# Kernel tuning notes

Measured on AMD Instinct MI355X. Metric: run time of the kernel, lower is better.

Reference implementation:

```python
import jax, jax.numpy as jnp
import numpy as np

NUM_USERS = 100000
NUM_ITEMS = 50000
D = 64
NUM_LAYERS = 2
NNZ_H = 3200000
NNZ_I = 3000000
EPS = 1e-12


def setup_inputs() -> dict:
    key = jax.random.key(0)
    ks = jax.random.split(key, 24)
    inp = {}
    inp['user_emb'] = jax.random.normal(ks[0], (NUM_USERS, D), jnp.float32) * 0.1
    inp['item_emb'] = jax.random.normal(ks[1], (NUM_ITEMS, D), jnp.float32) * 0.1
    inp['gating_w'] = jax.random.normal(ks[2], (4, D, D), jnp.float32) * 0.1
    inp['gating_b'] = jax.random.normal(ks[3], (4, 1, D), jnp.float32) * 0.1
    inp['sgating_w'] = jax.random.normal(ks[4], (3, D, D), jnp.float32) * 0.1
    inp['sgating_b'] = jax.random.normal(ks[5], (3, 1, D), jnp.float32) * 0.1
    inp['att_mat'] = jax.random.normal(ks[6], (D, D), jnp.float32) * 0.1
    inp['att_agg'] = jax.random.normal(ks[7], (1, D), jnp.float32) * 0.1
    inp['hs_row'] = jax.random.randint(ks[8], (NNZ_H,), 0, NUM_USERS, jnp.int32)
    inp['hs_col'] = jax.random.randint(ks[9], (NNZ_H,), 0, NUM_USERS, jnp.int32)
    inp['hs_val'] = jax.random.uniform(ks[10], (NNZ_H,), jnp.float32) / 32.0
    inp['hj_row'] = jax.random.randint(ks[11], (NNZ_H,), 0, NUM_USERS, jnp.int32)
    inp['hj_col'] = jax.random.randint(ks[12], (NNZ_H,), 0, NUM_USERS, jnp.int32)
    inp['hj_val'] = jax.random.uniform(ks[13], (NNZ_H,), jnp.float32) / 32.0
    inp['hp_row'] = jax.random.randint(ks[14], (NNZ_H,), 0, NUM_USERS, jnp.int32)
    inp['hp_col'] = jax.random.randint(ks[15], (NNZ_H,), 0, NUM_USERS, jnp.int32)
    inp['hp_val'] = jax.random.uniform(ks[16], (NNZ_H,), jnp.float32) / 32.0
    inp['inter_row'] = jax.random.randint(ks[17], (NNZ_I,), 0, NUM_USERS, jnp.int32)
    inp['inter_col'] = jax.random.randint(ks[18], (NNZ_I,), 0, NUM_ITEMS, jnp.int32)
    inp['inter_val'] = jax.random.uniform(ks[19], (NNZ_I,), jnp.float32) / 32.0
    return inp


def spmm(row, col, val, x, n_rows):
    # sparse (n_rows x m) @ dense (m x d), COO edges
    return jax.ops.segment_sum(val[:, None] * x[col], row, num_segments=n_rows)


def l2norm(x):
    return x / jnp.maximum(jnp.linalg.norm(x, axis=1, keepdims=True), EPS)


def self_gating(em, w, b):
    return em * jax.nn.sigmoid(em @ w + b)


def channel_attention(embs, att_mat, att_agg):
    # embs: list of 3 arrays [N, D]
    w = jnp.stack([jnp.sum(att_agg * (e @ att_mat), axis=1) for e in embs])  # [3, N]
    score = jax.nn.softmax(w, axis=0)
    mixed = score[0][:, None] * embs[0] + score[1][:, None] * embs[1] + score[2][:, None] * embs[2]
    return mixed, score


def reference(user_emb, item_emb, gating_w, gating_b, sgating_w, sgating_b,
              att_mat, att_agg,
              hs_row, hs_col, hs_val, hj_row, hj_col, hj_val,
              hp_row, hp_col, hp_val, inter_row, inter_col, inter_val):
    u_c0 = self_gating(user_emb, gating_w[0], gating_b[0])
    u_c1 = self_gating(user_emb, gating_w[1], gating_b[1])
    u_c2 = self_gating(user_emb, gating_w[2], gating_b[2])
    u_simple = self_gating(user_emb, gating_w[3], gating_b[3])
    it = item_emb
    acc_c0, acc_c1, acc_c2 = u_c0, u_c1, u_c2
    acc_simple, acc_item = u_simple, it
    for _ in range(NUM_LAYERS):
        mixed, _ = channel_attention([u_c0, u_c1, u_c2], att_mat, att_agg)
        mixed = (mixed + u_simple) / 2.0
        u_c0 = spmm(hs_row, hs_col, hs_val, u_c0, NUM_USERS)
        acc_c0 = acc_c0 + l2norm(u_c0)
        u_c1 = spmm(hj_row, hj_col, hj_val, u_c1, NUM_USERS)
        acc_c1 = acc_c1 + l2norm(u_c1)
        u_c2 = spmm(hp_row, hp_col, hp_val, u_c2, NUM_USERS)
        acc_c2 = acc_c2 + l2norm(u_c2)
        new_item = spmm(inter_col, inter_row, inter_val, mixed, NUM_ITEMS)  # inter^T @ mixed
        acc_item = acc_item + l2norm(new_item)
        u_simple = spmm(inter_row, inter_col, inter_val, it, NUM_USERS)  # inter @ item (old)
        acc_simple = acc_simple + l2norm(u_simple)
        it = new_item
    final_user, _ = channel_attention([acc_c0, acc_c1, acc_c2], att_mat, att_agg)
    final_user = final_user + acc_simple / 2.0
    sg0 = self_gating(final_user, sgating_w[0], sgating_b[0])
    sg1 = self_gating(final_user, sgating_w[1], sgating_b[1])
    sg2 = self_gating(final_user, sgating_w[2], sgating_b[2])
    return final_user, acc_item, sg0, sg1, sg2
```

## Files before the change

kernel.cpp:

```cpp
#include <hip/hip_runtime.h>

#define D 64
#define EPS 1e-12f

#define SB 6
#define BSZ (1 << SB)
#define NBMAX 2048
#define NCHUNK 128

__device__ __forceinline__ float wave_sum(float v) {
#pragma unroll
  for (int off = 32; off > 0; off >>= 1) v += __shfl_xor(v, off, 64);
  return v;
}

__global__ void compute_v_kernel(const float* __restrict__ att_mat,
                                 const float* __restrict__ att_agg,
                                 float* __restrict__ v) {
  int d = threadIdx.x;
  float s = 0.f;
#pragma unroll
  for (int j = 0; j < D; ++j) s += att_mat[d * D + j] * att_agg[j];
  v[d] = s;
}

__global__ __launch_bounds__(256) void gating4_kernel(
    const float* __restrict__ emb, const float* __restrict__ W,
    const float* __restrict__ B, float* __restrict__ u0, float* __restrict__ u1,
    float* __restrict__ u2, float* __restrict__ u3, float* __restrict__ a0,
    float* __restrict__ a1, float* __restrict__ a2, float* __restrict__ a3,
    int nrows) {
  __shared__ float sW[4 * D * D];
  for (int i = threadIdx.x; i < 4 * D * D; i += blockDim.x) sW[i] = W[i];
  __syncthreads();
  int lane = threadIdx.x & 63;
  int wid = (blockIdx.x * blockDim.x + threadIdx.x) >> 6;
  int nw = (gridDim.x * blockDim.x) >> 6;
  float b0 = B[0 * D + lane], b1 = B[1 * D + lane];
  float b2 = B[2 * D + lane], b3 = B[3 * D + lane];
  for (int r = wid; r < nrows; r += nw) {
    float e = emb[r * D + lane];
    float y0 = b0, y1 = b1, y2 = b2, y3 = b3;
#pragma unroll 16
    for (int j = 0; j < D; ++j) {
      float ej = __shfl(e, j, 64);
      y0 += ej * sW[0 * D * D + j * D + lane];
      y1 += ej * sW[1 * D * D + j * D + lane];
      y2 += ej * sW[2 * D * D + j * D + lane];
      y3 += ej * sW[3 * D * D + j * D + lane];
    }
    float o0 = e / (1.f + __expf(-y0));
    float o1 = e / (1.f + __expf(-y1));
    float o2 = e / (1.f + __expf(-y2));
    float o3 = e / (1.f + __expf(-y3));
    int idx = r * D + lane;
    u0[idx] = o0; a0[idx] = o0;
    u1[idx] = o1; a1[idx] = o1;
    u2[idx] = o2; a2[idx] = o2;
    u3[idx] = o3; a3[idx] = o3;
  }
}

__global__ __launch_bounds__(256) void sgating3_kernel(
    const float* __restrict__ x, const float* __restrict__ W,
    const float* __restrict__ B, float* __restrict__ o0f,
    float* __restrict__ o1f, float* __restrict__ o2f, int nrows) {
  __shared__ float sW[3 * D * D];
  for (int i = threadIdx.x; i < 3 * D * D; i += blockDim.x) sW[i] = W[i];
  __syncthreads();
  int lane = threadIdx.x & 63;
  int wid = (blockIdx.x * blockDim.x + threadIdx.x) >> 6;
  int nw = (gridDim.x * blockDim.x) >> 6;
  float b0 = B[0 * D + lane], b1 = B[1 * D + lane], b2 = B[2 * D + lane];
  for (int r = wid; r < nrows; r += nw) {
    float e = x[r * D + lane];
    float y0 = b0, y1 = b1, y2 = b2;
#pragma unroll 16
    for (int j = 0; j < D; ++j) {
      float ej = __shfl(e, j, 64);
      y0 += ej * sW[0 * D * D + j * D + lane];
      y1 += ej * sW[1 * D * D + j * D + lane];
      y2 += ej * sW[2 * D * D + j * D + lane];
    }
    int idx = r * D + lane;
    o0f[idx] = e / (1.f + __expf(-y0));
    o1f[idx] = e / (1.f + __expf(-y1));
    o2f[idx] = e / (1.f + __expf(-y2));
  }
}

__global__ __launch_bounds__(256) void attn_mix_kernel(
    const float* __restrict__ u0, const float* __restrict__ u1,
    const float* __restrict__ u2, const float* __restrict__ us,
    const float* __restrict__ v, float* __restrict__ mixed, int nrows) {
  int lane = threadIdx.x & 63;
  int wid = (blockIdx.x * blockDim.x + threadIdx.x) >> 6;
  if (wid >= nrows) return;
  int idx = wid * D + lane;
  float e0 = u0[idx], e1 = u1[idx], e2 = u2[idx], eu = us[idx];
  float vd = v[lane];
  float w0 = wave_sum(e0 * vd);
  float w1 = wave_sum(e1 * vd);
  float w2 = wave_sum(e2 * vd);
  float m = fmaxf(w0, fmaxf(w1, w2));
  float s0 = __expf(w0 - m), s1 = __expf(w1 - m), s2 = __expf(w2 - m);
  float inv = 1.f / (s0 + s1 + s2);
  mixed[idx] = ((s0 * e0 + s1 * e1 + s2 * e2) * inv + eu) * 0.5f;
}

__global__ __launch_bounds__(256) void final_attn_kernel(
    const float* __restrict__ a0, const float* __restrict__ a1,
    const float* __restrict__ a2, const float* __restrict__ as,
    const float* __restrict__ v, float* __restrict__ out, int nrows) {
  int lane = threadIdx.x & 63;
  int wid = (blockIdx.x * blockDim.x + threadIdx.x) >> 6;
  if (wid >= nrows) return;
  int idx = wid * D + lane;
  float e0 = a0[idx], e1 = a1[idx], e2 = a2[idx], eu = as[idx];
  float vd = v[lane];
  float w0 = wave_sum(e0 * vd);
  float w1 = wave_sum(e1 * vd);
  float w2 = wave_sum(e2 * vd);
  float m = fmaxf(w0, fmaxf(w1, w2));
  float s0 = __expf(w0 - m), s1 = __expf(w1 - m), s2 = __expf(w2 - m);
  float inv = 1.f / (s0 + s1 + s2);
  out[idx] = (s0 * e0 + s1 * e1 + s2 * e2) * inv + 0.5f * eu;
}

__global__ __launch_bounds__(256) void l2acc_kernel(const float* __restrict__ x,
                                                    float* __restrict__ acc,
                                                    int nrows) {
  int lane = threadIdx.x & 63;
  int wid = (blockIdx.x * blockDim.x + threadIdx.x) >> 6;
  if (wid >= nrows) return;
  int idx = wid * D + lane;
  float xv = x[idx];
  float ss = wave_sum(xv * xv);
  float nrm = fmaxf(sqrtf(ss), EPS);
  acc[idx] += xv / nrm;
}

__global__ __launch_bounds__(256) void spmm_atomic_kernel(
    const int* __restrict__ row, const int* __restrict__ col,
    const float* __restrict__ val, const float* __restrict__ x,
    float* __restrict__ out, int nnz) {
  int lane = threadIdx.x & 63;
  int wid = (blockIdx.x * blockDim.x + threadIdx.x) >> 6;
  int nw = (gridDim.x * blockDim.x) >> 6;
  for (int base = wid * 64; base < nnz; base += nw * 64) {
    int e = base + lane;
    int r = 0, c = 0;
    float v = 0.f;
    if (e < nnz) { r = row[e]; c = col[e]; v = val[e]; }
    int cnt = nnz - base; if (cnt > 64) cnt = 64;
    for (int i = 0; i < cnt; ++i) {
      int ri = __shfl(r, i, 64);
      int ci = __shfl(c, i, 64);
      float vi = __shfl(v, i, 64);
      float xv = x[ci * D + lane];
      atomicAdd(&out[ri * D + lane], vi * xv);
    }
  }
}


__global__ __launch_bounds__(256) void hist_kernel(const int* __restrict__ row,
                                                   int* __restrict__ counts,
                                                   int nnz) {
  int i = blockIdx.x * blockDim.x + threadIdx.x;
  int n = gridDim.x * blockDim.x;
  for (; i < nnz; i += n) atomicAdd(&counts[row[i]], 1);
}

__global__ __launch_bounds__(256) void scan1_kernel(const int* __restrict__ in,
                                                    int* __restrict__ out,
                                                    int* __restrict__ partials,
                                                    int n) {
  __shared__ int lds[256];
  int t = threadIdx.x;
  int base = blockIdx.x * 2048 + t * 8;
  int v[8];
  int s = 0;
#pragma unroll
  for (int k = 0; k < 8; ++k) {
    int i = base + k;
    v[k] = (i < n) ? in[i] : 0;
    s += v[k];
  }
  lds[t] = s;
  __syncthreads();
  for (int ofs = 1; ofs < 256; ofs <<= 1) {
    int add = 0;
    if (t >= ofs) add = lds[t - ofs];
    __syncthreads();
    if (t >= ofs) lds[t] += add;
    __syncthreads();
  }
  int excl = lds[t] - s;
  if (t == 255) partials[blockIdx.x] = lds[255];
  int run = excl;
#pragma unroll
  for (int k = 0; k < 8; ++k) {
    int i = base + k;
    if (i < n) out[i] = run;
    run += v[k];
  }
}

__global__ __launch_bounds__(256) void scan2_kernel(int* __restrict__ partials,
                                                    int P) {
  __shared__ int lds[256];
  int t = threadIdx.x;
  int s = (t < P) ? partials[t] : 0;
  lds[t] = s;
  __syncthreads();
  for (int ofs = 1; ofs < 256; ofs <<= 1) {
    int add = 0;
    if (t >= ofs) add = lds[t - ofs];
    __syncthreads();
    if (t >= ofs) lds[t] += add;
    __syncthreads();
  }
  if (t < P) partials[t] = lds[t] - s;
}

__global__ __launch_bounds__(256) void scan3_kernel(
    int* __restrict__ out, const int* __restrict__ partials, int n) {
  int i = blockIdx.x * blockDim.x + threadIdx.x;
  int nt = gridDim.x * blockDim.x;
  for (; i < n; i += nt) out[i] += partials[i >> 11];
}

__global__ __launch_bounds__(256) void bhist_kernel(
    const int* __restrict__ row, int* __restrict__ bh, int nnz, int nb,
    int chunk) {
  __shared__ int hist[NBMAX];
  for (int i = threadIdx.x; i < nb; i += blockDim.x) hist[i] = 0;
  __syncthreads();
  int base = blockIdx.x * chunk;
  int lim = base + chunk;
  if (lim > nnz) lim = nnz;
  for (int e = base + threadIdx.x; e < lim; e += blockDim.x)
    atomicAdd(&hist[row[e] >> SB], 1);
  __syncthreads();
  int* o = bh + blockIdx.x * nb;
  for (int i = threadIdx.x; i < nb; i += blockDim.x) o[i] = hist[i];
}

__global__ __launch_bounds__(256) void bscan_kernel(
    const int* __restrict__ row_ptr, int* __restrict__ bh, int nb) {
  int b = blockIdx.x * blockDim.x + threadIdx.x;
  if (b >= nb) return;
  int run = row_ptr[b << SB];
#pragma unroll 4
  for (int k = 0; k < NCHUNK; ++k) {
    int idx = k * nb + b;
    int t = bh[idx];
    bh[idx] = run;
    run += t;
  }
}

__global__ __launch_bounds__(256) void bscatter_kernel(
    const int* __restrict__ row, const int* __restrict__ col,
    const float* __restrict__ val, const int* __restrict__ bh,
    int2* __restrict__ staging, int nnz, int nb, int chunk) {
  __shared__ int cur[NBMAX];
  const int* o = bh + blockIdx.x * nb;
  for (int i = threadIdx.x; i < nb; i += blockDim.x) cur[i] = o[i];
  __syncthreads();
  int base = blockIdx.x * chunk;
  int lim = base + chunk;
  if (lim > nnz) lim = nnz;
  for (int e = base + threadIdx.x; e < lim; e += blockDim.x) {
    int r = row[e];
    int b = r >> SB;
    int idx = atomicAdd(&cur[b], 1);
    staging[idx] =
        make_int2(((r & (BSZ - 1)) << 24) | col[e], __float_as_int(val[e]));
  }
}

__global__ __launch_bounds__(256) void bucket_scatter_kernel(
    const int* __restrict__ row_ptr, const int2* __restrict__ staging,
    int2* __restrict__ edges_out, int nrows) {
  __shared__ int lfill[BSZ];
  int b = blockIdx.x;
  int r0 = b << SB;
  int t = threadIdx.x;
  int rend = r0 + BSZ;
  if (rend > nrows) rend = nrows;
  if (t < BSZ) {
    int r = r0 + t;
    lfill[t] = row_ptr[r < nrows ? r : nrows];
  }
  int bstart = row_ptr[r0];
  int bend = row_ptr[rend];
  __syncthreads();
  for (int e = bstart + t; e < bend; e += blockDim.x) {
    int2 ev = staging[e];
    int lrow = ((unsigned)ev.x) >> 24;
    int idx = atomicAdd(&lfill[lrow], 1);
    edges_out[idx] = make_int2(ev.x & 0xFFFFFF, ev.y);
  }
}

__global__ __launch_bounds__(256) void spmm_csr_l2acc_kernel(
    const int* __restrict__ row_ptr, const int2* __restrict__ edges,
    const float* __restrict__ x, float* __restrict__ out,
    float* __restrict__ acc, int nrows) {
  int lane = threadIdx.x & 63;
  int r = (blockIdx.x * blockDim.x + threadIdx.x) >> 6;
  if (r >= nrows) return;
  int start = row_ptr[r], end = row_ptr[r + 1];
  float sum = 0.f;
  for (int j = start; j < end; j += 64) {
    int e = j + lane;
    int c = 0;
    float v = 0.f;
    if (e < end) {
      int2 ev = edges[e];
      c = ev.x;
      v = __int_as_float(ev.y);
    }
    int cnt = end - j;
    if (cnt > 64) cnt = 64;
    int i = 0;
    for (; i + 4 <= cnt; i += 4) {
      int c0 = __shfl(c, i, 64);
      int c1 = __shfl(c, i + 1, 64);
      int c2 = __shfl(c, i + 2, 64);
      int c3 = __shfl(c, i + 3, 64);
      float v0 = __shfl(v, i, 64);
      float v1 = __shfl(v, i + 1, 64);
      float v2 = __shfl(v, i + 2, 64);
      float v3 = __shfl(v, i + 3, 64);
      float x0 = x[c0 * D + lane];
      float x1 = x[c1 * D + lane];
      float x2 = x[c2 * D + lane];
      float x3 = x[c3 * D + lane];
      sum += v0 * x0;
      sum += v1 * x1;
      sum += v2 * x2;
      sum += v3 * x3;
    }
    for (; i < cnt; ++i) {
      int ci = __shfl(c, i, 64);
      float vi = __shfl(v, i, 64);
      sum += vi * x[ci * D + lane];
    }
  }
  int idx = r * D + lane;
  out[idx] = sum;
  float ss = wave_sum(sum * sum);
  float nrm = fmaxf(sqrtf(ss), EPS);
  acc[idx] += sum / nrm;
}


static void build_csr(const int* row, const int* col, const float* val, int nnz,
                      int nrows, int* counts, int* row_ptr, int* partials,
                      int* bh, int2* staging, int2* edges_out,
                      hipStream_t stream) {
  int n1 = nrows + 1;
  hipMemsetAsync(counts, 0, n1 * sizeof(int), stream);
  hipLaunchKernelGGL(hist_kernel, dim3(1024), dim3(256), 0, stream, row, counts,
                     nnz);
  int nblk = (n1 + 2047) / 2048;
  hipLaunchKernelGGL(scan1_kernel, dim3(nblk), dim3(256), 0, stream, counts,
                     row_ptr, partials, n1);
  hipLaunchKernelGGL(scan2_kernel, dim3(1), dim3(256), 0, stream, partials,
                     nblk);
  hipLaunchKernelGGL(scan3_kernel, dim3(64), dim3(256), 0, stream, row_ptr,
                     partials, n1);
  int nb = (nrows + BSZ - 1) >> SB;
  int chunk = (nnz + NCHUNK - 1) / NCHUNK;
  hipLaunchKernelGGL(bhist_kernel, dim3(NCHUNK), dim3(256), 0, stream, row, bh,
                     nnz, nb, chunk);
  hipLaunchKernelGGL(bscan_kernel, dim3((nb + 255) / 256), dim3(256), 0, stream,
                     row_ptr, bh, nb);
  hipLaunchKernelGGL(bscatter_kernel, dim3(NCHUNK), dim3(256), 0, stream, row,
                     col, val, bh, staging, nnz, nb, chunk);
  hipLaunchKernelGGL(bucket_scatter_kernel, dim3(nb), dim3(256), 0, stream,
                     row_ptr, staging, edges_out, nrows);
}

extern "C" void kernel_launch(void* const* d_in, const int* in_sizes, int n_in,
                              void* d_out, int out_size, void* d_ws,
                              size_t ws_size, hipStream_t stream) {
  const float* user_emb = (const float*)d_in[0];
  const float* item_emb = (const float*)d_in[1];
  const float* gating_w = (const float*)d_in[2];
  const float* gating_b = (const float*)d_in[3];
  const float* sgating_w = (const float*)d_in[4];
  const float* sgating_b = (const float*)d_in[5];
  const float* att_mat = (const float*)d_in[6];
  const float* att_agg = (const float*)d_in[7];
  const int* hs_row = (const int*)d_in[8];
  const int* hs_col = (const int*)d_in[9];
  const float* hs_val = (const float*)d_in[10];
  const int* hj_row = (const int*)d_in[11];
  const int* hj_col = (const int*)d_in[12];
  const float* hj_val = (const float*)d_in[13];
  const int* hp_row = (const int*)d_in[14];
  const int* hp_col = (const int*)d_in[15];
  const float* hp_val = (const float*)d_in[16];
  const int* inter_row = (const int*)d_in[17];
  const int* inter_col = (const int*)d_in[18];
  const float* inter_val = (const float*)d_in[19];

  const int U = in_sizes[0] / D;
  const int I = in_sizes[1] / D;
  const int NH = in_sizes[8];
  const int NI = in_sizes[17];
  const size_t UD = (size_t)U * D;
  const size_t ID = (size_t)I * D;

  float* out = (float*)d_out;
  float* final_user = out;
  float* acc_item = out + UD;
  float* sg0 = out + UD + ID;
  float* sg1 = sg0 + UD;
  float* sg2 = sg1 + UD;
  float* acc0 = sg0, *acc1 = sg1, *acc2 = sg2, *accS = final_user;

  char* p = (char*)d_ws;
  auto alloc = [&](size_t bytes) -> void* {
    void* r = (void*)p;
    p += (bytes + 255) & ~(size_t)255;
    return r;
  };
  float* u0 = (float*)alloc(UD * 4);
  float* u1 = (float*)alloc(UD * 4);
  float* u2 = (float*)alloc(UD * 4);
  float* us = (float*)alloc(UD * 4);
  float* mixed = (float*)alloc(UD * 4);
  float* spare = (float*)alloc(UD * 4);
  float* it_a = (float*)alloc(ID * 4);
  float* it_b = (float*)alloc(ID * 4);
  float* v = (float*)alloc(256 * 4);
  int* partials = (int*)alloc(256 * 4);
  int* cnt_u = (int*)alloc((U + 2) * 4);
  int* cnt_i = (int*)alloc((I + 2) * 4);
  int* bh = (int*)alloc((size_t)NCHUNK * NBMAX * 4);
  int* rp_hs = (int*)alloc((U + 2) * 4);
  int* rp_hj = (int*)alloc((U + 2) * 4);
  int* rp_hp = (int*)alloc((U + 2) * 4);
  int* rp_iu = (int*)alloc((U + 2) * 4);
  int* rp_ii = (int*)alloc((I + 2) * 4);
  size_t NMAX = (size_t)(NH > NI ? NH : NI);
  int2* staging;
  if (NMAX * 8 <= UD * 4) staging = (int2*)spare;
  else staging = (int2*)alloc(NMAX * 8);
  int2* ed_hs = (int2*)alloc((size_t)NH * 8);
  int2* ed_hj = (int2*)alloc((size_t)NH * 8);
  int2* ed_hp = (int2*)alloc((size_t)NH * 8);
  int2* ed_iu = (int2*)alloc((size_t)NI * 8);
  int2* ed_ii = (int2*)alloc((size_t)NI * 8);
  size_t needed = (size_t)(p - (char*)d_ws);
  bool use_csr = needed <= ws_size && U < (1 << 24) && I < (1 << 24) &&
                 U <= NBMAX * BSZ && I <= NBMAX * BSZ;

  const int ROWB_U = (U + 3) / 4;
  const int ROWB_I = (I + 3) / 4;
  const int SPMM_BLOCKS = 2048;

  hipLaunchKernelGGL(compute_v_kernel, dim3(1), dim3(64), 0, stream, att_mat,
                     att_agg, v);
  hipLaunchKernelGGL(gating4_kernel, dim3(512), dim3(256), 0, stream, user_emb,
                     gating_w, gating_b, u0, u1, u2, us, acc0, acc1, acc2, accS,
                     U);
  hipMemcpyAsync(acc_item, item_emb, ID * sizeof(float),
                 hipMemcpyDeviceToDevice, stream);
  hipMemcpyAsync(it_a, item_emb, ID * sizeof(float), hipMemcpyDeviceToDevice,
                 stream);

  if (use_csr) {
    build_csr(hs_row, hs_col, hs_val, NH, U, cnt_u, rp_hs, partials, bh,
              staging, ed_hs, stream);
    build_csr(hj_row, hj_col, hj_val, NH, U, cnt_u, rp_hj, partials, bh,
              staging, ed_hj, stream);
    build_csr(hp_row, hp_col, hp_val, NH, U, cnt_u, rp_hp, partials, bh,
              staging, ed_hp, stream);
    build_csr(inter_row, inter_col, inter_val, NI, U, cnt_u, rp_iu, partials,
              bh, staging, ed_iu, stream);
    build_csr(inter_col, inter_row, inter_val, NI, I, cnt_i, rp_ii, partials,
              bh, staging, ed_ii, stream);
  }

  float* it_old = it_a;
  float* it_new = it_b;

  for (int layer = 0; layer < 2; ++layer) {
    hipLaunchKernelGGL(attn_mix_kernel, dim3(ROWB_U), dim3(256), 0, stream, u0,
                       u1, u2, us, v, mixed, U);
    if (use_csr) {
      hipLaunchKernelGGL(spmm_csr_l2acc_kernel, dim3(ROWB_U), dim3(256), 0,
                         stream, rp_hs, ed_hs, u0, spare, acc0, U);
      { float* t = u0; u0 = spare; spare = t; }
      hipLaunchKernelGGL(spmm_csr_l2acc_kernel, dim3(ROWB_U), dim3(256), 0,
                         stream, rp_hj, ed_hj, u1, spare, acc1, U);
      { float* t = u1; u1 = spare; spare = t; }
      hipLaunchKernelGGL(spmm_csr_l2acc_kernel, dim3(ROWB_U), dim3(256), 0,
                         stream, rp_hp, ed_hp, u2, spare, acc2, U);
      { float* t = u2; u2 = spare; spare = t; }
      hipLaunchKernelGGL(spmm_csr_l2acc_kernel, dim3(ROWB_I), dim3(256), 0,
                         stream, rp_ii, ed_ii, mixed, it_new, acc_item, I);
      hipLaunchKernelGGL(spmm_csr_l2acc_kernel, dim3(ROWB_U), dim3(256), 0,
                         stream, rp_iu, ed_iu, it_old, spare, accS, U);
      { float* t = us; us = spare; spare = t; }
    } else {
      hipMemsetAsync(spare, 0, UD * sizeof(float), stream);
      hipLaunchKernelGGL(spmm_atomic_kernel, dim3(SPMM_BLOCKS), dim3(256), 0,
                         stream, hs_row, hs_col, hs_val, u0, spare, NH);
      hipLaunchKernelGGL(l2acc_kernel, dim3(ROWB_U), dim3(256), 0, stream,
                         spare, acc0, U);
      { float* t = u0; u0 = spare; spare = t; }
      hipMemsetAsync(spare, 0, UD * sizeof(float), stream);
      hipLaunchKernelGGL(spmm_atomic_kernel, dim3(SPMM_BLOCKS), dim3(256), 0,
                         stream, hj_row, hj_col, hj_val, u1, spare, NH);
      hipLaunchKernelGGL(l2acc_kernel, dim3(ROWB_U), dim3(256), 0, stream,
                         spare, acc1, U);
      { float* t = u1; u1 = spare; spare = t; }
      hipMemsetAsync(spare, 0, UD * sizeof(float), stream);
      hipLaunchKernelGGL(spmm_atomic_kernel, dim3(SPMM_BLOCKS), dim3(256), 0,
                         stream, hp_row, hp_col, hp_val, u2, spare, NH);
      hipLaunchKernelGGL(l2acc_kernel, dim3(ROWB_U), dim3(256), 0, stream,
                         spare, acc2, U);
      { float* t = u2; u2 = spare; spare = t; }
      hipMemsetAsync(it_new, 0, ID * sizeof(float), stream);
      hipLaunchKernelGGL(spmm_atomic_kernel, dim3(SPMM_BLOCKS), dim3(256), 0,
                         stream, inter_col, inter_row, inter_val, mixed, it_new,
                         NI);
      hipLaunchKernelGGL(l2acc_kernel, dim3(ROWB_I), dim3(256), 0, stream,
                         it_new, acc_item, I);
      hipMemsetAsync(spare, 0, UD * sizeof(float), stream);
      hipLaunchKernelGGL(spmm_atomic_kernel, dim3(SPMM_BLOCKS), dim3(256), 0,
                         stream, inter_row, inter_col, inter_val, it_old, spare,
                         NI);
      hipLaunchKernelGGL(l2acc_kernel, dim3(ROWB_U), dim3(256), 0, stream,
                         spare, accS, U);
      { float* t = us; us = spare; spare = t; }
    }
    { float* t = it_old; it_old = it_new; it_new = t; }
  }

  hipLaunchKernelGGL(final_attn_kernel, dim3(ROWB_U), dim3(256), 0, stream,
                     acc0, acc1, acc2, accS, v, final_user, U);
  hipLaunchKernelGGL(sgating3_kernel, dim3(512), dim3(256), 0, stream,
                     final_user, sgating_w, sgating_b, sg0, sg1, sg2, U);
}
```

Before: 3.434 ms.

## Batch gating rows with float4 weights and skip accumulator init copies

The gating and self-gating kernels now process four rows per wave and keep the weight matrices interleaved as float4 in shared memory. This amortises each LDS weight read across rows and gates. On the CSR path the accumulator initial copies and the item-embedding memcpys are removed: the first-layer SpMM reads its base value directly from the initial embeddings instead of from pre-filled acc buffers. This saves several full-array writes and reads, at the cost of more registers per thread in the gating kernels and extra pointer plumbing for the item ping-pong buffers.

After: 3.281 ms. 4.4% less time.

```diff
diff --git a/kernel.cpp b/kernel.cpp
--- a/kernel.cpp
+++ b/kernel.cpp
@@ -30,34 +30,50 @@
     float* __restrict__ u2, float* __restrict__ u3, float* __restrict__ a0,
     float* __restrict__ a1, float* __restrict__ a2, float* __restrict__ a3,
     int nrows) {
-  __shared__ float sW[4 * D * D];
-  for (int i = threadIdx.x; i < 4 * D * D; i += blockDim.x) sW[i] = W[i];
+  __shared__ float4 sW4[D * D];
+  for (int i = threadIdx.x; i < D * D; i += blockDim.x)
+    sW4[i] = make_float4(W[i], W[D * D + i], W[2 * D * D + i],
+                         W[3 * D * D + i]);
   __syncthreads();
   int lane = threadIdx.x & 63;
   int wid = (blockIdx.x * blockDim.x + threadIdx.x) >> 6;
   int nw = (gridDim.x * blockDim.x) >> 6;
   float b0 = B[0 * D + lane], b1 = B[1 * D + lane];
   float b2 = B[2 * D + lane], b3 = B[3 * D + lane];
-  for (int r = wid; r < nrows; r += nw) {
-    float e = emb[r * D + lane];
-    float y0 = b0, y1 = b1, y2 = b2, y3 = b3;
+  for (int r0 = wid * 4; r0 < nrows; r0 += nw * 4) {
+    float e[4];
+    float y[4][4];
+#pragma unroll
+    for (int i = 0; i < 4; ++i) {
+      int r = r0 + i < nrows ? r0 + i : r0;
+      e[i] = emb[(size_t)r * D + lane];
+      y[i][0] = b0; y[i][1] = b1; y[i][2] = b2; y[i][3] = b3;
+    }
 #pragma unroll 16
     for (int j = 0; j < D; ++j) {
-      float ej = __shfl(e, j, 64);
-      y0 += ej * sW[0 * D * D + j * D + lane];
-      y1 += ej * sW[1 * D * D + j * D + lane];
-      y2 += ej * sW[2 * D * D + j * D + lane];
-      y3 += ej * sW[3 * D * D + j * D + lane];
-    }
-    float o0 = e / (1.f + __expf(-y0));
-    float o1 = e / (1.f + __expf(-y1));
-    float o2 = e / (1.f + __expf(-y2));
-    float o3 = e / (1.f + __expf(-y3));
-    int idx = r * D + lane;
-    u0[idx] = o0; a0[idx] = o0;
-    u1[idx] = o1; a1[idx] = o1;
-    u2[idx] = o2; a2[idx] = o2;
-    u3[idx] = o3; a3[idx] = o3;
+      float4 w = sW4[j * D + lane];
+#pragma unroll
+      for (int i = 0; i < 4; ++i) {
+        float ej = __shfl(e[i], j, 64);
+        y[i][0] += ej * w.x;
+        y[i][1] += ej * w.y;
+        y[i][2] += ej * w.z;
+        y[i][3] += ej * w.w;
+      }
+    }
+#pragma unroll
+    for (int i = 0; i < 4; ++i) {
+      int r = r0 + i;
+      if (r < nrows) {
+        size_t idx = (size_t)r * D + lane;
+        float o0 = e[i] / (1.f + __expf(-y[i][0]));
+        float o1 = e[i] / (1.f + __expf(-y[i][1]));
+        float o2 = e[i] / (1.f + __expf(-y[i][2]));
+        float o3 = e[i] / (1.f + __expf(-y[i][3]));
+        u0[idx] = o0; u1[idx] = o1; u2[idx] = o2; u3[idx] = o3;
+        if (a0) { a0[idx] = o0; a1[idx] = o1; a2[idx] = o2; a3[idx] = o3; }
+      }
+    }
   }
 }
 
@@ -65,27 +81,44 @@
     const float* __restrict__ x, const float* __restrict__ W,
     const float* __restrict__ B, float* __restrict__ o0f,
     float* __restrict__ o1f, float* __restrict__ o2f, int nrows) {
-  __shared__ float sW[3 * D * D];
-  for (int i = threadIdx.x; i < 3 * D * D; i += blockDim.x) sW[i] = W[i];
+  __shared__ float4 sW4[D * D];
+  for (int i = threadIdx.x; i < D * D; i += blockDim.x)
+    sW4[i] = make_float4(W[i], W[D * D + i], W[2 * D * D + i], 0.f);
   __syncthreads();
   int lane = threadIdx.x & 63;
   int wid = (blockIdx.x * blockDim.x + threadIdx.x) >> 6;
   int nw = (gridDim.x * blockDim.x) >> 6;
   float b0 = B[0 * D + lane], b1 = B[1 * D + lane], b2 = B[2 * D + lane];
-  for (int r = wid; r < nrows; r += nw) {
-    float e = x[r * D + lane];
-    float y0 = b0, y1 = b1, y2 = b2;
+  for (int r0 = wid * 4; r0 < nrows; r0 += nw * 4) {
+    float e[4];
+    float y[4][3];
+#pragma unroll
+    for (int i = 0; i < 4; ++i) {
+      int r = r0 + i < nrows ? r0 + i : r0;
+      e[i] = x[(size_t)r * D + lane];
+      y[i][0] = b0; y[i][1] = b1; y[i][2] = b2;
+    }
 #pragma unroll 16
     for (int j = 0; j < D; ++j) {
-      float ej = __shfl(e, j, 64);
-      y0 += ej * sW[0 * D * D + j * D + lane];
-      y1 += ej * sW[1 * D * D + j * D + lane];
-      y2 += ej * sW[2 * D * D + j * D + lane];
-    }
-    int idx = r * D + lane;
-    o0f[idx] = e / (1.f + __expf(-y0));
-    o1f[idx] = e / (1.f + __expf(-y1));
-    o2f[idx] = e / (1.f + __expf(-y2));
+      float4 w = sW4[j * D + lane];
+#pragma unroll
+      for (int i = 0; i < 4; ++i) {
+        float ej = __shfl(e[i], j, 64);
+        y[i][0] += ej * w.x;
+        y[i][1] += ej * w.y;
+        y[i][2] += ej * w.z;
+      }
+    }
+#pragma unroll
+    for (int i = 0; i < 4; ++i) {
+      int r = r0 + i;
+      if (r < nrows) {
+        size_t idx = (size_t)r * D + lane;
+        o0f[idx] = e[i] / (1.f + __expf(-y[i][0]));
+        o1f[idx] = e[i] / (1.f + __expf(-y[i][1]));
+        o2f[idx] = e[i] / (1.f + __expf(-y[i][2]));
+      }
+    }
   }
 }
 
@@ -308,7 +341,7 @@
 __global__ __launch_bounds__(256) void spmm_csr_l2acc_kernel(
     const int* __restrict__ row_ptr, const int2* __restrict__ edges,
     const float* __restrict__ x, float* __restrict__ out,
-    float* __restrict__ acc, int nrows) {
+    float* __restrict__ acc, const float* __restrict__ init, int nrows) {
   int lane = threadIdx.x & 63;
   int r = (blockIdx.x * blockDim.x + threadIdx.x) >> 6;
   if (r >= nrows) return;
@@ -354,7 +387,8 @@
   out[idx] = sum;
   float ss = wave_sum(sum * sum);
   float nrm = fmaxf(sqrtf(ss), EPS);
-  acc[idx] += sum / nrm;
+  float base = init ? init[idx] : acc[idx];
+  acc[idx] = base + sum / nrm;
 }
 
 
@@ -468,12 +502,17 @@
   hipLaunchKernelGGL(compute_v_kernel, dim3(1), dim3(64), 0, stream, att_mat,
                      att_agg, v);
   hipLaunchKernelGGL(gating4_kernel, dim3(512), dim3(256), 0, stream, user_emb,
-                     gating_w, gating_b, u0, u1, u2, us, acc0, acc1, acc2, accS,
-                     U);
-  hipMemcpyAsync(acc_item, item_emb, ID * sizeof(float),
-                 hipMemcpyDeviceToDevice, stream);
-  hipMemcpyAsync(it_a, item_emb, ID * sizeof(float), hipMemcpyDeviceToDevice,
-                 stream);
+                     gating_w, gating_b, u0, u1, u2, us,
+                     use_csr ? (float*)nullptr : acc0,
+                     use_csr ? (float*)nullptr : acc1,
+                     use_csr ? (float*)nullptr : acc2,
+                     use_csr ? (float*)nullptr : accS, U);
+  if (!use_csr) {
+    hipMemcpyAsync(acc_item, item_emb, ID * sizeof(float),
+                   hipMemcpyDeviceToDevice, stream);
+    hipMemcpyAsync(it_a, item_emb, ID * sizeof(float), hipMemcpyDeviceToDevice,
+                   stream);
+  }
 
   if (use_csr) {
     build_csr(hs_row, hs_col, hs_val, NH, U, cnt_u, rp_hs, partials, bh,
@@ -488,6 +527,8 @@
               bh, staging, ed_ii, stream);
   }
 
+  const float* it_src = item_emb;
+  float* it_dst = it_b;
   float* it_old = it_a;
   float* it_new = it_b;
 
@@ -495,20 +536,27 @@
     hipLaunchKernelGGL(attn_mix_kernel, dim3(ROWB_U), dim3(256), 0, stream, u0,
                        u1, u2, us, v, mixed, U);
     if (use_csr) {
+      const float* i0 = (layer == 0) ? u0 : nullptr;
+      const float* i1 = (layer == 0) ? u1 : nullptr;
+      const float* i2 = (layer == 0) ? u2 : nullptr;
+      const float* ii = (layer == 0) ? item_emb : nullptr;
+      const float* is = (layer == 0) ? us : nullptr;
       hipLaunchKernelGGL(spmm_csr_l2acc_kernel, dim3(ROWB_U), dim3(256), 0,
-                         stream, rp_hs, ed_hs, u0, spare, acc0, U);
+                         stream, rp_hs, ed_hs, u0, spare, acc0, i0, U);
       { float* t = u0; u0 = spare; spare = t; }
       hipLaunchKernelGGL(spmm_csr_l2acc_kernel, dim3(ROWB_U), dim3(256), 0,
-                         stream, rp_hj, ed_hj, u1, spare, acc1, U);
+                         stream, rp_hj, ed_hj, u1, spare, acc1, i1, U);
       { float* t = u1; u1 = spare; spare = t; }
       hipLaunchKernelGGL(spmm_csr_l2acc_kernel, dim3(ROWB_U), dim3(256), 0,
-                         stream, rp_hp, ed_hp, u2, spare, acc2, U);
+                         stream, rp_hp, ed_hp, u2, spare, acc2, i2, U);
       { float* t = u2; u2 = spare; spare = t; }
       hipLaunchKernelGGL(spmm_csr_l2acc_kernel, dim3(ROWB_I), dim3(256), 0,
-                         stream, rp_ii, ed_ii, mixed, it_new, acc_item, I);
+                         stream, rp_ii, ed_ii, mixed, it_dst, acc_item, ii, I);
       hipLaunchKernelGGL(spmm_csr_l2acc_kernel, dim3(ROWB_U), dim3(256), 0,
-                         stream, rp_iu, ed_iu, it_old, spare, accS, U);
+                         stream, rp_iu, ed_iu, it_src, spare, accS, is, U);
       { float* t = us; us = spare; spare = t; }
+      it_src = it_dst;
+      it_dst = it_a;
     } else {
       hipMemsetAsync(spare, 0, UD * sizeof(float), stream);
       hipLaunchKernelGGL(spmm_atomic_kernel, dim3(SPMM_BLOCKS), dim3(256), 0,
@@ -541,8 +589,8 @@
       hipLaunchKernelGGL(l2acc_kernel, dim3(ROWB_U), dim3(256), 0, stream,
                          spare, accS, U);
       { float* t = us; us = spare; spare = t; }
-    }
-    { float* t = it_old; it_old = it_new; it_new = t; }
+      { float* t = it_old; it_old = it_new; it_new = t; }
+    }
   }
 
   hipLaunchKernelGGL(final_attn_kernel, dim3(ROWB_U), dim3(256), 0, stream,
```
